# Performance work log

Measured on AMD Instinct MI355X. Metric: run time of the kernel, lower is better.

## Reference

```python
import jax, jax.numpy as jnp
import numpy as np

# ---- fixed problem dimensions ----
B, S, T = 64, 200, 32          # batch of sequences, trees per seq, nodes per tree
V, E, C = 50000, 128, 128      # vocab, embedding_dim, encode_dim
H, OUT = 100, 104              # GRU hidden, output_dim
N = B * S * T                  # total nodes
D_MAX = 5                      # max depth of a 32-node complete binary tree


def setup_inputs() -> dict:
    key = jax.random.key(0)
    ks = jax.random.split(key, 16)
    # --- tree structure: every tree is a complete binary tree with T nodes ---
    local_parent = np.array([0] + [(i - 1) // 2 for i in range(1, T)], dtype=np.int64)
    local_depth = np.array([int(np.floor(np.log2(i + 1))) for i in range(T)], dtype=np.int64)
    num_trees = B * S
    offsets = np.arange(num_trees, dtype=np.int64) * T
    node_parent = (offsets[:, None] + local_parent[None, :]).reshape(-1)
    node_depth = np.tile(local_depth, num_trees)
    node_tree = np.repeat(np.arange(num_trees, dtype=np.int64), T)
    node_tokens = jax.random.randint(ks[0], (N,), 0, V, dtype=jnp.int64)
    sc = 0.05
    inp = {
        "node_tokens": node_tokens,
        "node_parent": jnp.asarray(node_parent),
        "node_tree": jnp.asarray(node_tree),
        "node_depth": jnp.asarray(node_depth),
        "emb": jax.random.normal(ks[1], (V, E), jnp.float32) * sc,
        "w_lin": jax.random.normal(ks[2], (C, E), jnp.float32) * sc,
        "b_lin": jnp.zeros((C,), jnp.float32),
        "w_ih_f": jax.random.normal(ks[3], (3 * H, C), jnp.float32) * sc,
        "w_hh_f": jax.random.normal(ks[4], (3 * H, H), jnp.float32) * sc,
        "b_ih_f": jnp.zeros((3 * H,), jnp.float32),
        "b_hh_f": jnp.zeros((3 * H,), jnp.float32),
        "w_ih_b": jax.random.normal(ks[5], (3 * H, C), jnp.float32) * sc,
        "w_hh_b": jax.random.normal(ks[6], (3 * H, H), jnp.float32) * sc,
        "b_ih_b": jnp.zeros((3 * H,), jnp.float32),
        "b_hh_b": jnp.zeros((3 * H,), jnp.float32),
        "fc_w": jax.random.normal(ks[7], (OUT, 2 * H), jnp.float32) * sc,
        "fc_b": jnp.zeros((OUT,), jnp.float32),
    }
    return inp


def _gru(x_sbc, w_ih, w_hh, b_ih, b_hh):
    """Torch-convention GRU over leading time axis. x_sbc: [S, B, C] -> [S, B, H]."""
    h0 = jnp.zeros((x_sbc.shape[1], w_hh.shape[1]), x_sbc.dtype)

    def step(h, xt):
        gx = xt @ w_ih.T + b_ih
        gh = h @ w_hh.T + b_hh
        xr, xz, xn = jnp.split(gx, 3, axis=-1)
        hr, hz, hn = jnp.split(gh, 3, axis=-1)
        r = jax.nn.sigmoid(xr + hr)
        z = jax.nn.sigmoid(xz + hz)
        n = jnp.tanh(xn + r * hn)
        h_new = (1.0 - z) * n + z * h
        return h_new, h_new

    _, hs = jax.lax.scan(step, h0, x_sbc)
    return hs


def reference(node_tokens, node_parent, node_tree, node_depth,
              emb, w_lin, b_lin,
              w_ih_f, w_hh_f, b_ih_f, b_hh_f,
              w_ih_b, w_hh_b, b_ih_b, b_hh_b,
              fc_w, fc_b):
    # per-node contribution: W * emb(token) + b   (recursion base of hidden_state)
    c = emb[node_tokens] @ w_lin.T + b_lin               # [N, C]
    # level-batched bottom-up scatter-add: h(node) = c(node) + sum(h(children))
    h = c
    for d in range(D_MAX, 0, -1):
        mask = (node_depth == d)[:, None]
        h = h.at[node_parent].add(jnp.where(mask, h, 0.0))
    # per-tree max pool over all node hidden states (TreeEncoder output)
    tree_vec = jax.ops.segment_max(h, node_tree, num_segments=B * S)  # [B*S, C]
    x = tree_vec.reshape(B, S, C)
    # bidirectional GRU (batch_first in torch; scan over time here)
    x_t = jnp.transpose(x, (1, 0, 2))                    # [S, B, C]
    fwd = _gru(x_t, w_ih_f, w_hh_f, b_ih_f, b_hh_f)      # [S, B, H]
    bwd = _gru(x_t[::-1], w_ih_b, w_hh_b, b_ih_b, b_hh_b)[::-1]
    gru_out = jnp.concatenate([fwd, bwd], axis=-1)       # [S, B, 2H]
    pool = gru_out.max(axis=0)                           # [B, 2H] (max over time)
    return pool @ fc_w.T + fc_b                          # [B, OUT]
```

## Files before the change

### kernel.cpp

```cpp
#include <hip/hip_runtime.h>
#include <hip/hip_bf16.h>
#include <math.h>

#define BB 64
#define SS 200
#define TT 32
#define EE 128
#define CC 128
#define HH 100
#define G3 300
#define OUTD 104
#define NTREE (BB*SS)

typedef __attribute__((ext_vector_type(4))) float f32x4;
typedef _Float16 f16x8 __attribute__((ext_vector_type(8)));

__device__ inline float fast_sigmoid(float x) {
    return __builtin_amdgcn_rcpf(1.f + __builtin_amdgcn_exp2f(-1.4426950408889634f * x));
}
__device__ inline float fast_tanh(float x) {
    return 1.f - 2.f * __builtin_amdgcn_rcpf(1.f + __builtin_amdgcn_exp2f(2.8853900817779268f * x));
}

#define BAR() asm volatile("s_waitcnt lgkmcnt(0)\n\ts_barrier" ::: "memory")


__global__ __launch_bounds__(256) void k0_prep(const float* __restrict__ w_lin,
                                               const float* __restrict__ w_ih_f,
                                               const float* __restrict__ w_ih_b,
                                               _Float16* __restrict__ wl,
                                               _Float16* __restrict__ k2b) {
    const int tid  = threadIdx.x;
    const int wave = tid >> 6;
    const int lane = tid & 63;
    const int r = lane & 15;
    const int q = lane >> 4;
    if (blockIdx.x == 0) {
#pragma unroll
        for (int nt = 0; nt < 2; ++nt)
#pragma unroll
            for (int kt = 0; kt < 4; ++kt) {
                const int n = wave * 32 + nt * 16 + r;
                const float* src = w_lin + (long)n * EE + kt * 32 + q * 8;
                f16x8 f;
#pragma unroll
                for (int e = 0; e < 8; ++e) f[e] = (_Float16)src[e];
                *(f16x8*)&wl[(size_t)((((wave * 2 + nt) * 4 + kt) * 64) + lane) * 8] = f;
            }
    } else {
        const int nb = blockIdx.x - 1;
        const int n = nb * 64 + wave * 16 + r;
        const int dir = (n >= 320) ? 1 : 0;
        const int j = n - dir * 320;
        const int jj = (j < G3) ? j : 0;
        const float* w = dir ? w_ih_b : w_ih_f;
#pragma unroll
        for (int kt = 0; kt < 4; ++kt) {
            const float* src = w + (long)jj * EE + kt * 32 + q * 8;
            f16x8 f;
#pragma unroll
            for (int e = 0; e < 8; ++e) f[e] = (_Float16)src[e];
            *(f16x8*)&k2b[(size_t)((((nb * 4 + wave) * 4 + kt) * 64) + lane) * 8] = f;
        }
    }
}

#define K1_TPI 2
#define AROWS (K1_TPI*TT)
#define LDA 136
#define LDC 132

__global__ __launch_bounds__(256) void k1_mfma(const int* __restrict__ tok,
                                               const float* __restrict__ emb,
                                               const _Float16* __restrict__ wl,
                                               const float* __restrict__ b_lin,
                                               _Float16* __restrict__ thi) {
    __shared__ __align__(16) _Float16 A_sh[AROWS * LDA];
    __shared__ __align__(16) float C_sh[AROWS * LDC];
    __shared__ int tok_sh[AROWS];

    const int tid  = threadIdx.x;
    const int wave = tid >> 6;
    const int lane = tid & 63;
    const int r = lane & 15;
    const int q = lane >> 4;

    f16x8 bfrag[2][4];
    float bias[2];
#pragma unroll
    for (int nt = 0; nt < 2; ++nt) {
        bias[nt] = b_lin[wave * 32 + nt * 16 + r];
#pragma unroll
        for (int kt = 0; kt < 4; ++kt)
            bfrag[nt][kt] = *(const f16x8*)&wl[(size_t)((((wave * 2 + nt) * 4 + kt) * 64) + lane) * 8];
    }

    const int tree0 = blockIdx.x * K1_TPI;
    if (tid < AROWS) tok_sh[tid] = tok[tree0 * TT + tid];
    __syncthreads();

#pragma unroll
    for (int i = 0; i < 8; ++i) {
        const int idx = tid + i * 256;
        const int row = idx >> 5;
        const int p   = idx & 31;
        const float4 e = ((const float4*)(emb + (long)tok_sh[row] * EE))[p];
        _Float16* dst = &A_sh[row * LDA + p * 4];
        dst[0] = (_Float16)e.x; dst[1] = (_Float16)e.y;
        dst[2] = (_Float16)e.z; dst[3] = (_Float16)e.w;
    }
    __syncthreads();

    f32x4 acc[4][2];
#pragma unroll
    for (int mt = 0; mt < 4; ++mt)
#pragma unroll
        for (int nt = 0; nt < 2; ++nt) acc[mt][nt] = (f32x4)(0.f);

#pragma unroll
    for (int mt = 0; mt < 4; ++mt) {
        const int m = mt * 16 + r;
        f16x8 afrag[4];
#pragma unroll
        for (int kt = 0; kt < 4; ++kt)
            afrag[kt] = *(const f16x8*)&A_sh[m * LDA + kt * 32 + q * 8];
#pragma unroll
        for (int nt = 0; nt < 2; ++nt)
#pragma unroll
            for (int kt = 0; kt < 4; ++kt)
                acc[mt][nt] = __builtin_amdgcn_mfma_f32_16x16x32_f16(
                    afrag[kt], bfrag[nt][kt], acc[mt][nt], 0, 0, 0);
    }

#pragma unroll
    for (int mt = 0; mt < 4; ++mt)
#pragma unroll
        for (int nt = 0; nt < 2; ++nt) {
            const int col = wave * 32 + nt * 16 + r;
#pragma unroll
            for (int reg = 0; reg < 4; ++reg) {
                const int row = mt * 16 + q * 4 + reg;
                C_sh[row * LDC + col] = acc[mt][nt][reg] + bias[nt];
            }
        }
    __syncthreads();

    {
        const int t = tid >> 7;
        const int j = tid & 127;
        const float* base = &C_sh[(t * TT) * LDC + j];
        float v[TT];
#pragma unroll
        for (int n = 0; n < TT; ++n) v[n] = base[n * LDC];
        float mx = -1e30f;
#pragma unroll
        for (int n = TT - 1; n >= 1; --n) {
            mx = fmaxf(mx, v[n]);
            v[(n - 1) >> 1] += v[n];
        }
        mx = fmaxf(mx, v[0]);
        thi[(size_t)(tree0 + t) * CC + j] = (_Float16)mx;
    }
}

__global__ __launch_bounds__(256) void k2_mfma(const _Float16* __restrict__ thi,
                                               const _Float16* __restrict__ k2b,
                                               const float* __restrict__ b_ih_f,
                                               const float* __restrict__ b_ih_b,
                                               float* __restrict__ gx) {
    __shared__ __align__(16) _Float16 Ah[32 * LDA];

    const int tid  = threadIdx.x;
    const int wave = tid >> 6;
    const int lane = tid & 63;
    const int r = lane & 15;
    const int q = lane >> 4;

    const int nb = blockIdx.x % 10;
    const int mb = blockIdx.x / 10;
    const int m0 = mb * 32;
    const int n0 = nb * 64;

#pragma unroll
    for (int i = 0; i < 2; ++i) {
        const int idx = tid + i * 256;
        const int row = idx >> 4;
        const int p   = idx & 15;
        f16x8 v = *(const f16x8*)&thi[(size_t)(m0 + row) * CC + p * 8];
        *(f16x8*)&Ah[row * LDA + p * 8] = v;
    }
    f16x8 bh[4];
#pragma unroll
    for (int kt = 0; kt < 4; ++kt)
        bh[kt] = *(const f16x8*)&k2b[(size_t)((((nb * 4 + wave) * 4 + kt) * 64) + lane) * 8];
    __syncthreads();

    f32x4 acc[2];
    acc[0] = (f32x4)(0.f); acc[1] = (f32x4)(0.f);
#pragma unroll
    for (int mt = 0; mt < 2; ++mt) {
        const int m = mt * 16 + r;
#pragma unroll
        for (int kt = 0; kt < 4; ++kt) {
            f16x8 a = *(const f16x8*)&Ah[m * LDA + kt * 32 + q * 8];
            acc[mt] = __builtin_amdgcn_mfma_f32_16x16x32_f16(a, bh[kt], acc[mt], 0, 0, 0);
        }
    }

    const int ng  = n0 + wave * 16 + r;
    const int dir = (ng >= 320) ? 1 : 0;
    const int j   = ng - dir * 320;
    const bool valid = (j < G3);
    const float bias = valid ? (dir ? b_ih_b[j] : b_ih_f[j]) : 0.f;
    float* gxd = gx + (long)dir * NTREE * G3;
    if (valid) {
#pragma unroll
        for (int mt = 0; mt < 2; ++mt)
#pragma unroll
            for (int reg = 0; reg < 4; ++reg) {
                const int m = m0 + mt * 16 + q * 4 + reg;
                gxd[(long)m * G3 + j] = acc[mt][reg] + bias;
            }
    }
}

__global__ __launch_bounds__(256, 1) void k3_gru(const float* __restrict__ gx,
                                                 const float* __restrict__ w_hh_f,
                                                 const float* __restrict__ b_hh_f,
                                                 const float* __restrict__ w_hh_b,
                                                 const float* __restrict__ b_hh_b,
                                                 float* __restrict__ pool) {
    const int bid = blockIdx.x;
    const int dir = bid & 1;
    const int b = bid >> 1;
    const float* w_hh = dir ? w_hh_b : w_hh_f;
    const float* b_hh = dir ? b_hh_b : b_hh_f;

    __shared__ __align__(16) _Float16 h_sh[2][128];
    __shared__ float g_sh[4][80];

    const int tid  = threadIdx.x;
    const int wave = tid >> 6;
    const int lane = tid & 63;
    const int r = lane & 15;
    const int q = lane >> 4;

    f16x8 bf[5][4];
#pragma unroll
    for (int i = 0; i < 5; ++i) {
        const int l = i * 16 + r;
        const int gate = l / 25;
        const int ch   = l - gate * 25;
        const bool nv  = (l < 75);
        const int row  = gate * HH + wave * 25 + ch;
#pragma unroll
        for (int kt = 0; kt < 4; ++kt) {
            f16x8 f;
#pragma unroll
            for (int e = 0; e < 8; ++e) {
                const int k = kt * 32 + q * 8 + e;
                f[e] = (_Float16)((nv && k < HH) ? w_hh[row * HH + k] : 0.f);
            }
            bf[i][kt] = f;
        }
    }

    const int m = lane;
    const int c = wave * 25 + m;
    const bool act = (m < 25);
    float br = 0.f, bz = 0.f, bn = 0.f;
    if (act) { br = b_hh[c]; bz = b_hh[HH + c]; bn = b_hh[2 * HH + c]; }

    if (tid < 128) { h_sh[0][tid] = (_Float16)0.f; h_sh[1][tid] = (_Float16)0.f; }

    const float* gxd = gx + (long)dir * NTREE * G3;
    const int sstep = dir ? -1 : 1;
    int s = dir ? (SS - 1) : 0;
    float xr = 0.f, xz = 0.f, xn = 0.f;
    if (act) {
        const float* row0 = gxd + ((long)b * SS + s) * G3;
        xr = row0[c]; xz = row0[HH + c]; xn = row0[2 * HH + c];
    }
    float hj = 0.f, hmax = -1e30f;
    __syncthreads();

    for (int t = 0; t < SS; ++t) {
        const int p = t & 1;
        const int s_n = s + sstep;
        float xrn = 0.f, xzn = 0.f, xnn = 0.f;
        if (act && t < SS - 1) {
            const float* row0 = gxd + ((long)b * SS + s_n) * G3;
            xrn = row0[c]; xzn = row0[HH + c]; xnn = row0[2 * HH + c];
        }

        f16x8 a[4];
#pragma unroll
        for (int kt = 0; kt < 4; ++kt)
            a[kt] = *(const f16x8*)&h_sh[p][kt * 32 + q * 8];
        f32x4 acc[5];
#pragma unroll
        for (int i = 0; i < 5; ++i) {
            acc[i] = (f32x4)(0.f);
#pragma unroll
            for (int kt = 0; kt < 4; ++kt)
                acc[i] = __builtin_amdgcn_mfma_f32_16x16x32_f16(a[kt], bf[i][kt], acc[i], 0, 0, 0);
        }
        if (q == 0) {
#pragma unroll
            for (int i = 0; i < 5; ++i)
                g_sh[wave][i * 16 + r] = acc[i][0];
        }
        if (act) {
            const float ghr = g_sh[wave][m];
            const float ghz = g_sh[wave][25 + m];
            const float ghn = g_sh[wave][50 + m];
            const float rg = fast_sigmoid(xr + ghr + br);
            const float zg = fast_sigmoid(xz + ghz + bz);
            const float ng = fast_tanh(xn + rg * (ghn + bn));
            hj = (1.f - zg) * ng + zg * hj;
            hmax = fmaxf(hmax, hj);
            h_sh[1 - p][c] = (_Float16)hj;
            xr = xrn; xz = xzn; xn = xnn;
        }
        BAR();
        s = s_n;
    }
    if (act) pool[(long)b * (2 * HH) + dir * HH + c] = hmax;
}

__global__ __launch_bounds__(256) void k4_fc(const float* __restrict__ pool,
                                             const float* __restrict__ fc_w,
                                             const float* __restrict__ fc_b,
                                             float* __restrict__ out) {
    const int b = blockIdx.x;
    __shared__ __align__(16) float p_sh[2 * HH];
    const int t = threadIdx.x;
    if (t < 2 * HH) p_sh[t] = pool[(long)b * (2 * HH) + t];
    __syncthreads();
    if (t < OUTD) {
        const float4* wr4 = (const float4*)(fc_w + (long)t * (2 * HH));
        const float4* p4 = (const float4*)p_sh;
        float a0 = 0.f, a1 = 0.f;
#pragma unroll
        for (int k = 0; k < 50; k += 2) {
            float4 w0 = wr4[k],   p0 = p4[k];
            float4 w1 = wr4[k+1], p1 = p4[k+1];
            a0 += w0.x*p0.x + w0.y*p0.y + w0.z*p0.z + w0.w*p0.w;
            a1 += w1.x*p1.x + w1.y*p1.y + w1.z*p1.z + w1.w*p1.w;
        }
        out[(long)b * OUTD + t] = fc_b[t] + a0 + a1;
    }
}

extern "C" void kernel_launch(void* const* d_in, const int* in_sizes, int n_in,
                              void* d_out, int out_size, void* d_ws, size_t ws_size,
                              hipStream_t stream) {
    const int*   tok    = (const int*)d_in[0];
    const float* emb    = (const float*)d_in[4];
    const float* w_lin  = (const float*)d_in[5];
    const float* b_lin  = (const float*)d_in[6];
    const float* w_ih_f = (const float*)d_in[7];
    const float* w_hh_f = (const float*)d_in[8];
    const float* b_ih_f = (const float*)d_in[9];
    const float* b_hh_f = (const float*)d_in[10];
    const float* w_ih_b = (const float*)d_in[11];
    const float* w_hh_b = (const float*)d_in[12];
    const float* b_ih_b = (const float*)d_in[13];
    const float* b_hh_b = (const float*)d_in[14];
    const float* fc_w   = (const float*)d_in[15];
    const float* fc_b   = (const float*)d_in[16];

    char* wsb = (char*)d_ws;
    _Float16* wl   = (_Float16*)(wsb);
    _Float16* k2b  = (_Float16*)(wsb + 32768);
    _Float16* thi  = (_Float16*)(wsb + 196608);
    float*    gx   = (float*)(wsb + 3473408);
    float*    pool = (float*)(wsb);
    float*    out  = (float*)d_out;

    k0_prep<<<11, 256, 0, stream>>>(w_lin, w_ih_f, w_ih_b, wl, k2b);
    k1_mfma<<<NTREE / K1_TPI, 256, 0, stream>>>(tok, emb, wl, b_lin, thi);
    k2_mfma<<<(NTREE / 32) * 10, 256, 0, stream>>>(thi, k2b, b_ih_f, b_ih_b, gx);
    k3_gru <<<2 * BB, 256, 0, stream>>>(gx, w_hh_f, b_hh_f, w_hh_b, b_hh_b, pool);
    k4_fc  <<<BB, 256, 0, stream>>>(pool, fc_w, fc_b, out);
}
```

Measured before the change: 244.2 us.

## Pre-convert embedding table to fp16 and use shuffles in the GRU step

k0_prep gains 3125 extra blocks that convert the whole fp32 embedding table to fp16 in workspace, which overlaps the gx buffer. k1 then gathers half as many bytes per token. Separately, the GRU step splits the MFMA chain into two independent accumulators, prefetches gx two steps ahead, and replaces the shared-memory gate exchange with cross-lane shuffles. Converting the full 25.6 MB table on every call adds streaming traffic that may exceed what the smaller gather saves.

```diff
diff --git a/kernel.cpp b/kernel.cpp
--- a/kernel.cpp
+++ b/kernel.cpp
@@ -5,6 +5,7 @@
 #define BB 64
 #define SS 200
 #define TT 32
+#define VV 50000
 #define EE 128
 #define CC 128
 #define HH 100
@@ -28,8 +29,10 @@
 __global__ __launch_bounds__(256) void k0_prep(const float* __restrict__ w_lin,
                                                const float* __restrict__ w_ih_f,
                                                const float* __restrict__ w_ih_b,
+                                               const float* __restrict__ emb,
                                                _Float16* __restrict__ wl,
-                                               _Float16* __restrict__ k2b) {
+                                               _Float16* __restrict__ k2b,
+                                               _Float16* __restrict__ emb16) {
     const int tid  = threadIdx.x;
     const int wave = tid >> 6;
     const int lane = tid & 63;
@@ -47,7 +50,7 @@
                 for (int e = 0; e < 8; ++e) f[e] = (_Float16)src[e];
                 *(f16x8*)&wl[(size_t)((((wave * 2 + nt) * 4 + kt) * 64) + lane) * 8] = f;
             }
-    } else {
+    } else if (blockIdx.x <= 10) {
         const int nb = blockIdx.x - 1;
         const int n = nb * 64 + wave * 16 + r;
         const int dir = (n >= 320) ? 1 : 0;
@@ -62,6 +65,18 @@
             for (int e = 0; e < 8; ++e) f[e] = (_Float16)src[e];
             *(f16x8*)&k2b[(size_t)((((nb * 4 + wave) * 4 + kt) * 64) + lane) * 8] = f;
         }
+    } else {
+        const long base = (long)(blockIdx.x - 11) * 2048 + (long)tid * 8;
+        if (base < (long)VV * EE) {
+            const float4* s = (const float4*)(emb + base);
+            const float4 v0 = s[0], v1 = s[1];
+            f16x8 f;
+            f[0] = (_Float16)v0.x; f[1] = (_Float16)v0.y;
+            f[2] = (_Float16)v0.z; f[3] = (_Float16)v0.w;
+            f[4] = (_Float16)v1.x; f[5] = (_Float16)v1.y;
+            f[6] = (_Float16)v1.z; f[7] = (_Float16)v1.w;
+            *(f16x8*)&emb16[base] = f;
+        }
     }
 }
 
@@ -71,7 +86,7 @@
 #define LDC 132
 
 __global__ __launch_bounds__(256) void k1_mfma(const int* __restrict__ tok,
-                                               const float* __restrict__ emb,
+                                               const _Float16* __restrict__ emb16,
                                                const _Float16* __restrict__ wl,
                                                const float* __restrict__ b_lin,
                                                _Float16* __restrict__ thi) {
@@ -100,14 +115,12 @@
     __syncthreads();
 
 #pragma unroll
-    for (int i = 0; i < 8; ++i) {
+    for (int i = 0; i < 4; ++i) {
         const int idx = tid + i * 256;
-        const int row = idx >> 5;
-        const int p   = idx & 31;
-        const float4 e = ((const float4*)(emb + (long)tok_sh[row] * EE))[p];
-        _Float16* dst = &A_sh[row * LDA + p * 4];
-        dst[0] = (_Float16)e.x; dst[1] = (_Float16)e.y;
-        dst[2] = (_Float16)e.z; dst[3] = (_Float16)e.w;
+        const int row = idx >> 4;
+        const int p   = idx & 15;
+        const f16x8 v = *(const f16x8*)&emb16[(long)tok_sh[row] * EE + p * 8];
+        *(f16x8*)&A_sh[row * LDA + p * 8] = v;
     }
     __syncthreads();
 
@@ -237,7 +250,6 @@
     const float* b_hh = dir ? b_hh_b : b_hh_f;
 
     __shared__ __align__(16) _Float16 h_sh[2][128];
-    __shared__ float g_sh[4][80];
 
     const int tid  = threadIdx.x;
     const int wave = tid >> 6;
@@ -271,59 +283,77 @@
     float br = 0.f, bz = 0.f, bn = 0.f;
     if (act) { br = b_hh[c]; bz = b_hh[HH + c]; bn = b_hh[2 * HH + c]; }
 
+    const int a_z  = (25 + m) & 63;
+    const int a_n1 = (50 + m) & 63;
+    const int a_n2 = (50 + m - 64) & 63;
+    const bool nV1 = (50 + m) < 64;
+
     if (tid < 128) { h_sh[0][tid] = (_Float16)0.f; h_sh[1][tid] = (_Float16)0.f; }
 
     const float* gxd = gx + (long)dir * NTREE * G3;
     const int sstep = dir ? -1 : 1;
     int s = dir ? (SS - 1) : 0;
     float xr = 0.f, xz = 0.f, xn = 0.f;
+    float xr1 = 0.f, xz1 = 0.f, xn1 = 0.f;
     if (act) {
-        const float* row0 = gxd + ((long)b * SS + s) * G3;
-        xr = row0[c]; xz = row0[HH + c]; xn = row0[2 * HH + c];
+        const float* r0 = gxd + ((long)b * SS + s) * G3;
+        xr = r0[c]; xz = r0[HH + c]; xn = r0[2 * HH + c];
+        const float* r1 = gxd + ((long)b * SS + s + sstep) * G3;
+        xr1 = r1[c]; xz1 = r1[HH + c]; xn1 = r1[2 * HH + c];
     }
     float hj = 0.f, hmax = -1e30f;
     __syncthreads();
 
     for (int t = 0; t < SS; ++t) {
         const int p = t & 1;
-        const int s_n = s + sstep;
-        float xrn = 0.f, xzn = 0.f, xnn = 0.f;
-        if (act && t < SS - 1) {
-            const float* row0 = gxd + ((long)b * SS + s_n) * G3;
-            xrn = row0[c]; xzn = row0[HH + c]; xnn = row0[2 * HH + c];
+        float xr2 = 0.f, xz2 = 0.f, xn2 = 0.f;
+        if (act && t < SS - 2) {
+            const float* r2 = gxd + ((long)b * SS + (s + 2 * sstep)) * G3;
+            xr2 = r2[c]; xz2 = r2[HH + c]; xn2 = r2[2 * HH + c];
         }
 
         f16x8 a[4];
 #pragma unroll
         for (int kt = 0; kt < 4; ++kt)
             a[kt] = *(const f16x8*)&h_sh[p][kt * 32 + q * 8];
-        f32x4 acc[5];
+
+        f32x4 accA[5], accB[5];
 #pragma unroll
         for (int i = 0; i < 5; ++i) {
-            acc[i] = (f32x4)(0.f);
-#pragma unroll
-            for (int kt = 0; kt < 4; ++kt)
-                acc[i] = __builtin_amdgcn_mfma_f32_16x16x32_f16(a[kt], bf[i][kt], acc[i], 0, 0, 0);
-        }
-        if (q == 0) {
-#pragma unroll
-            for (int i = 0; i < 5; ++i)
-                g_sh[wave][i * 16 + r] = acc[i][0];
-        }
+            accA[i] = (f32x4)(0.f);
+            accB[i] = (f32x4)(0.f);
+            accA[i] = __builtin_amdgcn_mfma_f32_16x16x32_f16(a[0], bf[i][0], accA[i], 0, 0, 0);
+            accB[i] = __builtin_amdgcn_mfma_f32_16x16x32_f16(a[2], bf[i][2], accB[i], 0, 0, 0);
+            accA[i] = __builtin_amdgcn_mfma_f32_16x16x32_f16(a[1], bf[i][1], accA[i], 0, 0, 0);
+            accB[i] = __builtin_amdgcn_mfma_f32_16x16x32_f16(a[3], bf[i][3], accB[i], 0, 0, 0);
+        }
+        const float g0 = accA[0][0] + accB[0][0];
+        const float g1 = accA[1][0] + accB[1][0];
+        const float g2 = accA[2][0] + accB[2][0];
+        const float g3 = accA[3][0] + accB[3][0];
+        const float g4 = accA[4][0] + accB[4][0];
+        float V1 = g0;
+        V1 = (q == 1) ? g1 : V1;
+        V1 = (q == 2) ? g2 : V1;
+        V1 = (q == 3) ? g3 : V1;
+        const float ghr = V1;
+        const float ghz = __shfl(V1, a_z);
+        const float vnA = __shfl(V1, a_n1);
+        const float vnB = __shfl(g4, a_n2);
+        const float ghn = nV1 ? vnA : vnB;
+
         if (act) {
-            const float ghr = g_sh[wave][m];
-            const float ghz = g_sh[wave][25 + m];
-            const float ghn = g_sh[wave][50 + m];
             const float rg = fast_sigmoid(xr + ghr + br);
             const float zg = fast_sigmoid(xz + ghz + bz);
             const float ng = fast_tanh(xn + rg * (ghn + bn));
             hj = (1.f - zg) * ng + zg * hj;
+            h_sh[1 - p][c] = (_Float16)hj;
             hmax = fmaxf(hmax, hj);
-            h_sh[1 - p][c] = (_Float16)hj;
-            xr = xrn; xz = xzn; xn = xnn;
+            xr = xr1; xz = xz1; xn = xn1;
+            xr1 = xr2; xz1 = xz2; xn1 = xn2;
         }
         BAR();
-        s = s_n;
+        s += sstep;
     }
     if (act) pool[(long)b * (2 * HH) + dir * HH + c] = hmax;
 }
@@ -371,15 +401,16 @@
     const float* fc_b   = (const float*)d_in[16];
 
     char* wsb = (char*)d_ws;
-    _Float16* wl   = (_Float16*)(wsb);
-    _Float16* k2b  = (_Float16*)(wsb + 32768);
-    _Float16* thi  = (_Float16*)(wsb + 196608);
-    float*    gx   = (float*)(wsb + 3473408);
-    float*    pool = (float*)(wsb);
-    float*    out  = (float*)d_out;
-
-    k0_prep<<<11, 256, 0, stream>>>(w_lin, w_ih_f, w_ih_b, wl, k2b);
-    k1_mfma<<<NTREE / K1_TPI, 256, 0, stream>>>(tok, emb, wl, b_lin, thi);
+    _Float16* wl    = (_Float16*)(wsb);
+    _Float16* k2b   = (_Float16*)(wsb + 32768);
+    _Float16* thi   = (_Float16*)(wsb + 196608);
+    float*    gx    = (float*)(wsb + 3473408);
+    _Float16* emb16 = (_Float16*)(wsb + 3473408);
+    float*    pool  = (float*)(wsb);
+    float*    out   = (float*)d_out;
+
+    k0_prep<<<11 + 3125, 256, 0, stream>>>(w_lin, w_ih_f, w_ih_b, emb, wl, k2b, emb16);
+    k1_mfma<<<NTREE / K1_TPI, 256, 0, stream>>>(tok, emb16, wl, b_lin, thi);
     k2_mfma<<<(NTREE / 32) * 10, 256, 0, stream>>>(thi, k2b, b_ih_f, b_ih_b, gx);
     k3_gru <<<2 * BB, 256, 0, stream>>>(gx, w_hh_f, b_hh_f, w_hh_b, b_hh_b, pool);
     k4_fc  <<<BB, 256, 0, stream>>>(pool, fc_w, fc_b, out);
```

New measurement: 246.8 us. About the same (+1.1%).
